# Kernel optimization log

Hardware: AMD Instinct MI355X
Metric: run time of the kernel (lower is better)

## Reference

```python
import jax, jax.numpy as jnp
import numpy as np

N, IN_DIM, OUT_DIM, H = 4096, 128, 128, 4
HEAD_DIM = OUT_DIM // H
NEG_SLOPE = 0.2


def setup_inputs() -> dict:
    key = jax.random.key(0)
    k1, k2, k3, k4, k5 = jax.random.split(key, 5)
    x = jax.random.normal(k1, (N, IN_DIM), dtype=jnp.float32)
    adj = jax.random.randint(k2, (N, N), 0, 2, dtype=jnp.int32)
    # nn.Linear(in_dim, out_dim, bias=False): weight is [out_dim, in_dim]
    W = jax.random.normal(k3, (OUT_DIM, IN_DIM), dtype=jnp.float32) * (1.0 / np.sqrt(IN_DIM))
    attn_src = jax.random.normal(k4, (1, H, HEAD_DIM), dtype=jnp.float32) * 0.1
    attn_dst = jax.random.normal(k5, (1, H, HEAD_DIM), dtype=jnp.float32) * 0.1
    return {"x": x, "adj": adj, "W": W, "attn_src": attn_src, "attn_dst": attn_dst}


def reference(x, adj, W, attn_src, attn_dst):
    n = x.shape[0]
    h = (x @ W.T).reshape(n, H, HEAD_DIM)            # [N, H, D]
    e_src = jnp.sum(h * attn_src, axis=-1)           # [N, H]
    e_dst = jnp.sum(h * attn_dst, axis=-1)           # [N, H]
    e = e_src[:, None, :] + e_dst[None, :, :]        # [N, N, H]
    e = jax.nn.leaky_relu(e, negative_slope=NEG_SLOPE)
    e = jnp.where((adj == 0)[:, :, None], -jnp.inf, e)
    alpha = jax.nn.softmax(e, axis=1)                # softmax over neighbors j
    # dropout omitted (eval mode)
    out = jnp.einsum('ijh,jhd->ihd', alpha, h)       # [N, H, D]
    return out.reshape(n, -1)
```

## Files before the change

kernel.cpp:

```cpp
#include <hip/hip_runtime.h>
#include <hip/hip_bf16.h>

#define NN 4096
#define SJ 8
#define JCH (NN / SJ)
#define JSTEP 64
#define NSTEPS (JCH / JSTEP)
#define LOG2E 1.44269504f

typedef __attribute__((ext_vector_type(4))) float f32x4;
typedef __attribute__((ext_vector_type(4))) int i32x4;
typedef __attribute__((ext_vector_type(4))) unsigned int u32x4;
typedef __attribute__((ext_vector_type(8))) short short8;

__device__ __forceinline__ unsigned pk2(float a, float b) {
    float2 t; t.x = a; t.y = b;
    __hip_bfloat162 h = __float22bfloat162_rn(t);
    unsigned r;
    __builtin_memcpy(&r, &h, 4);
    return r;
}

__device__ __forceinline__ short8 load8_bf(const float* __restrict__ p) {
    f32x4 a = *(const f32x4*)p;
    f32x4 b = *(const f32x4*)(p + 4);
    u32x4 v = {pk2(a[0], a[1]), pk2(a[2], a[3]), pk2(b[0], b[1]), pk2(b[2], b[3])};
    return __builtin_bit_cast(short8, v);
}

__global__ __launch_bounds__(256) void k1_proj(
        const float* __restrict__ x, const float* __restrict__ W,
        const float* __restrict__ asrc, const float* __restrict__ adst,
        unsigned short* __restrict__ hT, float* __restrict__ Rt,
        unsigned* __restrict__ BDt) {
    __shared__ unsigned short ttile[4][32][16];
    const int ibase = blockIdx.x * 16;
    const int w = threadIdx.x >> 6;
    const int lane = threadIdx.x & 63;
    const int grp = lane >> 4, li = lane & 15;

    const float* xrow = x + (ibase + li) * 128;
    const float* w0 = W + (w * 32 + li) * 128;
    const float* w1 = W + (w * 32 + 16 + li) * 128;

    f32x4 c0 = {0.f, 0.f, 0.f, 0.f}, c1 = {0.f, 0.f, 0.f, 0.f};
#pragma unroll
    for (int ko = 0; ko < 128; ko += 32) {
        const int kk = ko + grp * 8;
        short8 a = load8_bf(xrow + kk);
        short8 b0 = load8_bf(w0 + kk);
        short8 b1 = load8_bf(w1 + kk);
        c0 = __builtin_amdgcn_mfma_f32_16x16x32_bf16(a, b0, c0, 0, 0, 0);
        c1 = __builtin_amdgcn_mfma_f32_16x16x32_bf16(a, b1, c1, 0, 0, 0);
    }
    const float as0 = asrc[w * 32 + li], as1 = asrc[w * 32 + 16 + li];
    const float ad0 = adst[w * 32 + li], ad1 = adst[w * 32 + 16 + li];
    float pes[4], ped[4];
#pragma unroll
    for (int r = 0; r < 4; ++r) {
        pes[r] = c0[r] * as0 + c1[r] * as1;
        ped[r] = c0[r] * ad0 + c1[r] * ad1;
    }
#pragma unroll
    for (int m = 1; m < 16; m <<= 1) {
#pragma unroll
        for (int r = 0; r < 4; ++r) {
            pes[r] += __shfl_xor(pes[r], m);
            ped[r] += __shfl_xor(ped[r], m);
        }
    }
    if (li == 0) {
#pragma unroll
        for (int r = 0; r < 4; ++r) {
            const int row = ibase + grp * 4 + r;
            Rt[w * NN + row] = __builtin_amdgcn_exp2f(-0.8f * LOG2E * pes[r]);
            const float Bv = __builtin_amdgcn_exp2f(LOG2E * ped[r]);
            const float Dv = __builtin_amdgcn_exp2f(0.2f * LOG2E * ped[r]);
            BDt[w * NN + row] = pk2(Bv, Dv);
        }
    }
    unsigned short* tw = &ttile[w][0][0];
    {
        uint2 v0; v0.x = pk2(c0[0], c0[1]); v0.y = pk2(c0[2], c0[3]);
        uint2 v1; v1.x = pk2(c1[0], c1[1]); v1.y = pk2(c1[2], c1[3]);
        *(uint2*)&tw[li * 16 + grp * 4] = v0;
        *(uint2*)&tw[(li + 16) * 16 + grp * 4] = v1;
    }
    __syncthreads();
    const int d = lane >> 1, half = lane & 1;
    u32x4 v = *(const u32x4*)&ttile[w][d][half * 8];
    *(u32x4*)(hT + (size_t)(w * 32 + d) * NN + ibase + half * 8) = v;
}

__device__ __forceinline__ u32x4 gld0(const void* p) {
    u32x4 d; asm volatile("global_load_dwordx4 %0, %1, off" : "=&v"(d) : "v"(p)); return d;
}
__device__ __forceinline__ u32x4 gld16(const void* p) {
    u32x4 d; asm volatile("global_load_dwordx4 %0, %1, off offset:16" : "=&v"(d) : "v"(p)); return d;
}
__device__ __forceinline__ u32x4 gld64(const void* p) {
    u32x4 d; asm volatile("global_load_dwordx4 %0, %1, off offset:64" : "=&v"(d) : "v"(p)); return d;
}
__device__ __forceinline__ u32x4 gld128(const void* p) {
    u32x4 d; asm volatile("global_load_dwordx4 %0, %1, off offset:128" : "=&v"(d) : "v"(p)); return d;
}
__device__ __forceinline__ u32x4 gld144(const void* p) {
    u32x4 d; asm volatile("global_load_dwordx4 %0, %1, off offset:144" : "=&v"(d) : "v"(p)); return d;
}

struct SR { u32x4 h0k0, h0k1, h1k0, h1k1, bd00, bd01, bd10, bd11; };

#define LOADR(dst, toff) do {                                             \
    (dst).h0k0 = gld0(h0b + (toff));  (dst).h0k1 = gld64(h0b + (toff));   \
    (dst).h1k0 = gld0(h1b + (toff));  (dst).h1k1 = gld64(h1b + (toff));   \
    (dst).bd00 = gld0(bd + (toff));   (dst).bd01 = gld16(bd + (toff));    \
    (dst).bd10 = gld128(bd + (toff)); (dst).bd11 = gld144(bd + (toff));   \
} while (0)

#define LAUNDER(s) asm volatile("" : "+v"((s).h0k0), "+v"((s).h0k1),      \
    "+v"((s).h1k0), "+v"((s).h1k1), "+v"((s).bd00), "+v"((s).bd01),       \
    "+v"((s).bd10), "+v"((s).bd11))

__device__ __forceinline__ short8 buildQ(float R, const u32x4 ba, const u32x4 bb,
                                         const i32x4 q0, const i32x4 q1) {
    float p[8];
#pragma unroll
    for (int e = 0; e < 4; ++e) {
        const unsigned v = ba[e];
        const float B = __builtin_bit_cast(float, v << 16);
        const float D = __builtin_bit_cast(float, v & 0xFFFF0000u);
        const float m = fmaxf(B, R * D);
        p[e] = __builtin_bit_cast(float, __builtin_bit_cast(unsigned, m) & (0u - (unsigned)q0[e]));
    }
#pragma unroll
    for (int e = 0; e < 4; ++e) {
        const unsigned v = bb[e];
        const float B = __builtin_bit_cast(float, v << 16);
        const float D = __builtin_bit_cast(float, v & 0xFFFF0000u);
        const float m = fmaxf(B, R * D);
        p[4 + e] = __builtin_bit_cast(float, __builtin_bit_cast(unsigned, m) & (0u - (unsigned)q1[e]));
    }
    u32x4 u = {pk2(p[0], p[1]), pk2(p[2], p[3]), pk2(p[4], p[5]), pk2(p[6], p[7])};
    return __builtin_bit_cast(short8, u);
}

__global__ __launch_bounds__(256) void k3_main(
        const int* __restrict__ adj, const unsigned short* __restrict__ hT,
        const float* __restrict__ Rt, const unsigned* __restrict__ BDt,
        float* __restrict__ numer, float* __restrict__ denom) {
    __shared__ unsigned int adjb[4][3][16 * 64];

    const int ibase = blockIdx.x * 16;
    const int jstart = blockIdx.y * JCH;
    const int head = threadIdx.x >> 6;
    const int lane = threadIdx.x & 63;
    const int grp = lane >> 4, li = lane & 15;
    const int sub = lane >> 4, p = lane & 15;

    const float R0 = Rt[head * NN + ibase + li];
    const unsigned short* h0b = hT + (size_t)(head * 32 + li) * NN + jstart + grp * 8;
    const unsigned short* h1b = h0b + (size_t)16 * NN;
    const unsigned* bd = BDt + head * NN + jstart + grp * 8;
    const unsigned int* adju = (const unsigned int*)adj;

    const unsigned int* g[4];
#pragma unroll
    for (int k = 0; k < 4; ++k) {
        const int r = k * 4 + sub;
        g[k] = adju + (size_t)(ibase + r) * NN + jstart + (p ^ (r & 15)) * 4;
    }

    f32x4 c0 = {0.f,0.f,0.f,0.f}, c1 = {0.f,0.f,0.f,0.f}, dn = {0.f,0.f,0.f,0.f};
    short8 bones;
#pragma unroll
    for (int e = 0; e < 8; ++e) bones[e] = (short)0x3F80;

    auto stage = [&](int slot, int s) {
#pragma unroll
        for (int k = 0; k < 4; ++k)
            __builtin_amdgcn_global_load_lds(g[k] + s * JSTEP,
                                             &adjb[head][slot][k * 4 * 64], 16, 0, 0);
    };
    auto compute = [&](const unsigned int* buf, const SR& S) {
#pragma unroll
        for (int ks = 0; ks < 2; ++ks) {
            const u32x4 ba = ks ? S.bd10 : S.bd00;
            const u32x4 bb = ks ? S.bd11 : S.bd01;
            const short8 tA = __builtin_bit_cast(short8, ks ? S.h0k1 : S.h0k0);
            const short8 tB = __builtin_bit_cast(short8, ks ? S.h1k1 : S.h1k0);
            const int cb = ks * 8 + grp * 2;
            const i32x4 q0 = *(const i32x4*)&buf[li * 64 + ((cb) ^ li) * 4];
            const i32x4 q1 = *(const i32x4*)&buf[li * 64 + ((cb + 1) ^ li) * 4];
            const short8 A = buildQ(R0, ba, bb, q0, q1);
            c0 = __builtin_amdgcn_mfma_f32_16x16x32_bf16(A, tA, c0, 0, 0, 0);
            c1 = __builtin_amdgcn_mfma_f32_16x16x32_bf16(A, tB, c1, 0, 0, 0);
            dn = __builtin_amdgcn_mfma_f32_16x16x32_bf16(A, bones, dn, 0, 0, 0);
        }
    };

    SR S0, S1;
    LOADR(S0, 0);
    __builtin_amdgcn_sched_barrier(0);
    stage(0, 0);
    __builtin_amdgcn_sched_barrier(0);
    stage(1, 1);
    __builtin_amdgcn_sched_barrier(0);
    asm volatile("s_waitcnt vmcnt(4)" ::: "memory");
    LAUNDER(S0);
    __builtin_amdgcn_sched_barrier(0);

#pragma unroll
    for (int t = 0; t < NSTEPS; ++t) {
        SR& Scur = (t & 1) ? S1 : S0;
        SR& Snxt = (t & 1) ? S0 : S1;
        if (t + 1 < NSTEPS) { LOADR(Snxt, (t + 1) * JSTEP); }
        __builtin_amdgcn_sched_barrier(0);
        if (t + 2 < NSTEPS) stage((t + 2) % 3, t + 2);
        __builtin_amdgcn_sched_barrier(0);

        compute(&adjb[head][t % 3][0], Scur);

        if (t + 1 < NSTEPS) {
            if (t + 2 < NSTEPS) {
                asm volatile("s_waitcnt vmcnt(4)" ::: "memory");
            } else {
                asm volatile("s_waitcnt vmcnt(0)" ::: "memory");
            }
            LAUNDER(Snxt);
            __builtin_amdgcn_sched_barrier(0);
        }
    }

    const int r0 = ibase + grp * 4;
    float* nb = numer + head * 32 + li;
#pragma unroll
    for (int r = 0; r < 4; ++r) {
        atomicAdd(nb + (size_t)(r0 + r) * 128, c0[r]);
        atomicAdd(nb + (size_t)(r0 + r) * 128 + 16, c1[r]);
    }
    if (li == 0) {
#pragma unroll
        for (int r = 0; r < 4; ++r)
            atomicAdd(denom + (r0 + r) * 4 + head, dn[r]);
    }
}

__global__ __launch_bounds__(256) void k4_fin(const float* __restrict__ numer,
                                              const float* __restrict__ denom,
                                              float* __restrict__ out) {
    const int idx = blockIdx.x * 256 + threadIdx.x;
    const int node = idx >> 7;
    const int headc = (idx & 127) >> 5;
    out[idx] = numer[idx] / denom[node * 4 + headc];
}

extern "C" void kernel_launch(void* const* d_in, const int* in_sizes, int n_in,
                              void* d_out, int out_size, void* d_ws, size_t ws_size,
                              hipStream_t stream) {
    const float* x = (const float*)d_in[0];
    const int* adj = (const int*)d_in[1];
    const float* W = (const float*)d_in[2];
    const float* asrc = (const float*)d_in[3];
    const float* adst = (const float*)d_in[4];
    float* out = (float*)d_out;

    char* ws = (char*)d_ws;
    float* numer = (float*)ws;
    float* denom = (float*)(ws + (size_t)2097152);
    float* Rt = (float*)(ws + (size_t)2097152 + 65536);
    unsigned* BDt = (unsigned*)(ws + (size_t)2097152 + 131072);
    unsigned short* hT = (unsigned short*)(ws + (size_t)2097152 + 196608);

    (void)hipMemsetAsync(numer, 0, 2097152 + 65536, stream);
    k1_proj<<<256, 256, 0, stream>>>(x, W, asrc, adst, hT, Rt, BDt);
    k3_main<<<dim3(256, SJ), 256, 0, stream>>>(adj, hT, Rt, BDt, numer, denom);
    k4_fin<<<2048, 256, 0, stream>>>(numer, denom, out);
}
```

Before: 70.38 us.

## Share adjacency tile across heads with 64-row blocks and block barriers

Each block now covers 64 destination rows instead of 16. All four head-waves share one LDS adjacency buffer, and each wave loops over four 16-row groups, so the per-head h/BD register loads are reused four times. Previously every head wave loaded the same 16 adjacency rows separately, so the adjacency traffic was duplicated across heads and h/BD was fetched per 16 rows. In exchange the kernel adds cross-wave s_barriers, four times more accumulators (register pressure), and a grid of only 512 blocks, which lowers occupancy and parallelism.

```diff
diff --git a/kernel.cpp b/kernel.cpp
--- a/kernel.cpp
+++ b/kernel.cpp
@@ -148,29 +148,37 @@
         const int* __restrict__ adj, const unsigned short* __restrict__ hT,
         const float* __restrict__ Rt, const unsigned* __restrict__ BDt,
         float* __restrict__ numer, float* __restrict__ denom) {
-    __shared__ unsigned int adjb[4][3][16 * 64];
-
-    const int ibase = blockIdx.x * 16;
+    __shared__ unsigned int adjb[3][64 * 64];
+
+    const int ibase = blockIdx.x * 64;
     const int jstart = blockIdx.y * JCH;
     const int head = threadIdx.x >> 6;
     const int lane = threadIdx.x & 63;
     const int grp = lane >> 4, li = lane & 15;
     const int sub = lane >> 4, p = lane & 15;
 
-    const float R0 = Rt[head * NN + ibase + li];
+    float Rv[4];
+#pragma unroll
+    for (int g = 0; g < 4; ++g) Rv[g] = Rt[head * NN + ibase + g * 16 + li];
     const unsigned short* h0b = hT + (size_t)(head * 32 + li) * NN + jstart + grp * 8;
     const unsigned short* h1b = h0b + (size_t)16 * NN;
     const unsigned* bd = BDt + head * NN + jstart + grp * 8;
     const unsigned int* adju = (const unsigned int*)adj;
 
-    const unsigned int* g[4];
+    const unsigned int* gs[4];
 #pragma unroll
     for (int k = 0; k < 4; ++k) {
-        const int r = k * 4 + sub;
-        g[k] = adju + (size_t)(ibase + r) * NN + jstart + (p ^ (r & 15)) * 4;
-    }
-
-    f32x4 c0 = {0.f,0.f,0.f,0.f}, c1 = {0.f,0.f,0.f,0.f}, dn = {0.f,0.f,0.f,0.f};
+        const int r = head * 16 + k * 4 + sub;
+        gs[k] = adju + (size_t)(ibase + r) * NN + jstart + (p ^ (r & 15)) * 4;
+    }
+
+    f32x4 c[4][2], dn[4];
+#pragma unroll
+    for (int g = 0; g < 4; ++g) {
+        c[g][0] = f32x4{0.f,0.f,0.f,0.f};
+        c[g][1] = f32x4{0.f,0.f,0.f,0.f};
+        dn[g] = f32x4{0.f,0.f,0.f,0.f};
+    }
     short8 bones;
 #pragma unroll
     for (int e = 0; e < 8; ++e) bones[e] = (short)0x3F80;
@@ -178,8 +186,8 @@
     auto stage = [&](int slot, int s) {
 #pragma unroll
         for (int k = 0; k < 4; ++k)
-            __builtin_amdgcn_global_load_lds(g[k] + s * JSTEP,
-                                             &adjb[head][slot][k * 4 * 64], 16, 0, 0);
+            __builtin_amdgcn_global_load_lds(gs[k] + s * JSTEP,
+                                             &adjb[slot][(head * 16 + k * 4) * 64], 16, 0, 0);
     };
     auto compute = [&](const unsigned int* buf, const SR& S) {
 #pragma unroll
@@ -189,24 +197,29 @@
             const short8 tA = __builtin_bit_cast(short8, ks ? S.h0k1 : S.h0k0);
             const short8 tB = __builtin_bit_cast(short8, ks ? S.h1k1 : S.h1k0);
             const int cb = ks * 8 + grp * 2;
-            const i32x4 q0 = *(const i32x4*)&buf[li * 64 + ((cb) ^ li) * 4];
-            const i32x4 q1 = *(const i32x4*)&buf[li * 64 + ((cb + 1) ^ li) * 4];
-            const short8 A = buildQ(R0, ba, bb, q0, q1);
-            c0 = __builtin_amdgcn_mfma_f32_16x16x32_bf16(A, tA, c0, 0, 0, 0);
-            c1 = __builtin_amdgcn_mfma_f32_16x16x32_bf16(A, tB, c1, 0, 0, 0);
-            dn = __builtin_amdgcn_mfma_f32_16x16x32_bf16(A, bones, dn, 0, 0, 0);
+#pragma unroll
+            for (int g = 0; g < 4; ++g) {
+                const int rr = g * 16 + li;
+                const i32x4 q0 = *(const i32x4*)&buf[rr * 64 + ((cb) ^ li) * 4];
+                const i32x4 q1 = *(const i32x4*)&buf[rr * 64 + ((cb + 1) ^ li) * 4];
+                const short8 A = buildQ(Rv[g], ba, bb, q0, q1);
+                c[g][0] = __builtin_amdgcn_mfma_f32_16x16x32_bf16(A, tA, c[g][0], 0, 0, 0);
+                c[g][1] = __builtin_amdgcn_mfma_f32_16x16x32_bf16(A, tB, c[g][1], 0, 0, 0);
+                dn[g] = __builtin_amdgcn_mfma_f32_16x16x32_bf16(A, bones, dn[g], 0, 0, 0);
+            }
         }
     };
 
     SR S0, S1;
+    stage(0, 0);
+    __builtin_amdgcn_sched_barrier(0);
     LOADR(S0, 0);
-    __builtin_amdgcn_sched_barrier(0);
-    stage(0, 0);
     __builtin_amdgcn_sched_barrier(0);
     stage(1, 1);
     __builtin_amdgcn_sched_barrier(0);
     asm volatile("s_waitcnt vmcnt(4)" ::: "memory");
     LAUNDER(S0);
+    __builtin_amdgcn_s_barrier();
     __builtin_amdgcn_sched_barrier(0);
 
 #pragma unroll
@@ -218,7 +231,7 @@
         if (t + 2 < NSTEPS) stage((t + 2) % 3, t + 2);
         __builtin_amdgcn_sched_barrier(0);
 
-        compute(&adjb[head][t % 3][0], Scur);
+        compute(&adjb[t % 3][0], Scur);
 
         if (t + 1 < NSTEPS) {
             if (t + 2 < NSTEPS) {
@@ -227,21 +240,29 @@
                 asm volatile("s_waitcnt vmcnt(0)" ::: "memory");
             }
             LAUNDER(Snxt);
+            __builtin_amdgcn_s_barrier();
             __builtin_amdgcn_sched_barrier(0);
         }
     }
 
-    const int r0 = ibase + grp * 4;
     float* nb = numer + head * 32 + li;
 #pragma unroll
-    for (int r = 0; r < 4; ++r) {
-        atomicAdd(nb + (size_t)(r0 + r) * 128, c0[r]);
-        atomicAdd(nb + (size_t)(r0 + r) * 128 + 16, c1[r]);
+    for (int g = 0; g < 4; ++g) {
+        const int r0 = ibase + g * 16 + grp * 4;
+#pragma unroll
+        for (int r = 0; r < 4; ++r) {
+            atomicAdd(nb + (size_t)(r0 + r) * 128, c[g][0][r]);
+            atomicAdd(nb + (size_t)(r0 + r) * 128 + 16, c[g][1][r]);
+        }
     }
     if (li == 0) {
 #pragma unroll
-        for (int r = 0; r < 4; ++r)
-            atomicAdd(denom + (r0 + r) * 4 + head, dn[r]);
+        for (int g = 0; g < 4; ++g) {
+            const int r0 = ibase + g * 16 + grp * 4;
+#pragma unroll
+            for (int r = 0; r < 4; ++r)
+                atomicAdd(denom + (r0 + r) * 4 + head, dn[g][r]);
+        }
     }
 }
 
@@ -273,6 +294,6 @@
 
     (void)hipMemsetAsync(numer, 0, 2097152 + 65536, stream);
     k1_proj<<<256, 256, 0, stream>>>(x, W, asrc, adst, hT, Rt, BDt);
-    k3_main<<<dim3(256, SJ), 256, 0, stream>>>(adj, hT, Rt, BDt, numer, denom);
+    k3_main<<<dim3(64, SJ), 256, 0, stream>>>(adj, hT, Rt, BDt, numer, denom);
     k4_fin<<<2048, 256, 0, stream>>>(numer, denom, out);
 }
```

Measured after the change: 59.75 us. 15.1% less time.

## Split heads into single-wave blocks and deepen register prefetch to three buffers

Applied to the files above, without the earlier changes.

The main kernel now launches one 64-thread block per head, row tile and j-chunk instead of four heads per 256-thread block. Each block holds its own three-slot LDS adjacency buffer. Register-held BD/hT operands are now prefetched two steps ahead with a triple-buffered rotation, and the wait counts are adjusted to match, so global latency is hidden deeper. The cost is that each head-block reloads the same adjacency tile (adjacency traffic becomes four times larger, though L2 may absorb it), register pressure rises, and there are more, smaller blocks.

```diff
diff --git a/kernel.cpp b/kernel.cpp
--- a/kernel.cpp
+++ b/kernel.cpp
@@ -144,16 +144,16 @@
     return __builtin_bit_cast(short8, u);
 }
 
-__global__ __launch_bounds__(256) void k3_main(
+__global__ __launch_bounds__(64) void k3_main(
         const int* __restrict__ adj, const unsigned short* __restrict__ hT,
         const float* __restrict__ Rt, const unsigned* __restrict__ BDt,
         float* __restrict__ numer, float* __restrict__ denom) {
-    __shared__ unsigned int adjb[4][3][16 * 64];
-
-    const int ibase = blockIdx.x * 16;
-    const int jstart = blockIdx.y * JCH;
-    const int head = threadIdx.x >> 6;
-    const int lane = threadIdx.x & 63;
+    __shared__ unsigned int adjb[3][16 * 64];
+
+    const int head = blockIdx.x;
+    const int ibase = blockIdx.y * 16;
+    const int jstart = blockIdx.z * JCH;
+    const int lane = threadIdx.x;
     const int grp = lane >> 4, li = lane & 15;
     const int sub = lane >> 4, p = lane & 15;
 
@@ -163,11 +163,11 @@
     const unsigned* bd = BDt + head * NN + jstart + grp * 8;
     const unsigned int* adju = (const unsigned int*)adj;
 
-    const unsigned int* g[4];
+    const unsigned int* gs[4];
 #pragma unroll
     for (int k = 0; k < 4; ++k) {
         const int r = k * 4 + sub;
-        g[k] = adju + (size_t)(ibase + r) * NN + jstart + (p ^ (r & 15)) * 4;
+        gs[k] = adju + (size_t)(ibase + r) * NN + jstart + (p ^ (r & 15)) * 4;
     }
 
     f32x4 c0 = {0.f,0.f,0.f,0.f}, c1 = {0.f,0.f,0.f,0.f}, dn = {0.f,0.f,0.f,0.f};
@@ -178,8 +178,8 @@
     auto stage = [&](int slot, int s) {
 #pragma unroll
         for (int k = 0; k < 4; ++k)
-            __builtin_amdgcn_global_load_lds(g[k] + s * JSTEP,
-                                             &adjb[head][slot][k * 4 * 64], 16, 0, 0);
+            __builtin_amdgcn_global_load_lds(gs[k] + s * JSTEP,
+                                             &adjb[slot][k * 4 * 64], 16, 0, 0);
     };
     auto compute = [&](const unsigned int* buf, const SR& S) {
 #pragma unroll
@@ -198,38 +198,48 @@
         }
     };
 
-    SR S0, S1;
+    SR S0, S1, S2;
+
+#define STEP(T, CUR, NXT, FAR) do {                                            \
+    if ((T) + 2 < NSTEPS) {                                                    \
+        stage(((T) + 2) % 3, (T) + 2);                                         \
+        __builtin_amdgcn_sched_barrier(0);                                     \
+        LOADR(FAR, ((T) + 2) * JSTEP);                                         \
+        __builtin_amdgcn_sched_barrier(0);                                     \
+    }                                                                          \
+    compute(&adjb[(T) % 3][0], CUR);                                           \
+    if ((T) + 1 < NSTEPS) {                                                    \
+        if ((T) + 2 < NSTEPS) {                                                \
+            asm volatile("s_waitcnt vmcnt(12)" ::: "memory");                  \
+        } else {                                                               \
+            asm volatile("s_waitcnt vmcnt(0)" ::: "memory");                   \
+        }                                                                      \
+        LAUNDER(NXT);                                                          \
+        __builtin_amdgcn_sched_barrier(0);                                     \
+    }                                                                          \
+} while (0)
+
+    stage(0, 0);
+    __builtin_amdgcn_sched_barrier(0);
     LOADR(S0, 0);
     __builtin_amdgcn_sched_barrier(0);
-    stage(0, 0);
-    __builtin_amdgcn_sched_barrier(0);
     stage(1, 1);
     __builtin_amdgcn_sched_barrier(0);
-    asm volatile("s_waitcnt vmcnt(4)" ::: "memory");
+    LOADR(S1, JSTEP);
+    __builtin_amdgcn_sched_barrier(0);
+    asm volatile("s_waitcnt vmcnt(12)" ::: "memory");
     LAUNDER(S0);
     __builtin_amdgcn_sched_barrier(0);
 
-#pragma unroll
-    for (int t = 0; t < NSTEPS; ++t) {
-        SR& Scur = (t & 1) ? S1 : S0;
-        SR& Snxt = (t & 1) ? S0 : S1;
-        if (t + 1 < NSTEPS) { LOADR(Snxt, (t + 1) * JSTEP); }
-        __builtin_amdgcn_sched_barrier(0);
-        if (t + 2 < NSTEPS) stage((t + 2) % 3, t + 2);
-        __builtin_amdgcn_sched_barrier(0);
-
-        compute(&adjb[head][t % 3][0], Scur);
-
-        if (t + 1 < NSTEPS) {
-            if (t + 2 < NSTEPS) {
-                asm volatile("s_waitcnt vmcnt(4)" ::: "memory");
-            } else {
-                asm volatile("s_waitcnt vmcnt(0)" ::: "memory");
-            }
-            LAUNDER(Snxt);
-            __builtin_amdgcn_sched_barrier(0);
-        }
-    }
+    STEP(0, S0, S1, S2);
+    STEP(1, S1, S2, S0);
+    STEP(2, S2, S0, S1);
+    STEP(3, S0, S1, S2);
+    STEP(4, S1, S2, S0);
+    STEP(5, S2, S0, S1);
+    STEP(6, S0, S1, S2);
+    STEP(7, S1, S2, S0);
+#undef STEP
 
     const int r0 = ibase + grp * 4;
     float* nb = numer + head * 32 + li;
@@ -273,6 +283,6 @@
 
     (void)hipMemsetAsync(numer, 0, 2097152 + 65536, stream);
     k1_proj<<<256, 256, 0, stream>>>(x, W, asrc, adst, hT, Rt, BDt);
-    k3_main<<<dim3(256, SJ), 256, 0, stream>>>(adj, hT, Rt, BDt, numer, denom);
+    k3_main<<<dim3(4, 256, SJ), 64, 0, stream>>>(adj, hT, Rt, BDt, numer, denom);
     k4_fin<<<2048, 256, 0, stream>>>(numer, denom, out);
 }
```

New measurement: 70.59 us. Within noise of the previous version (+0.3%).
